# Optimization experiments

Measured on AMD Instinct MI355X. Metric: run time of the kernel, lower is better.

## Reference

```python
import jax, jax.numpy as jnp
import numpy as np

DEGREE = 7

def setup_inputs() -> dict:
    key = jax.random.key(0)
    k1, k2 = jax.random.split(key)
    input_dims, output_dims = 1024, 1024
    x = jax.random.normal(k1, (8192, input_dims), dtype=jnp.float32)
    std = 1.0 / (input_dims * (DEGREE + 1))
    lucas_coeffs = std * jax.random.normal(k2, (input_dims, output_dims, DEGREE + 1), dtype=jnp.float32)
    return {"x": x, "lucas_coeffs": lucas_coeffs}

def reference(x, lucas_coeffs):
    input_dims = lucas_coeffs.shape[0]
    x = x.reshape(-1, input_dims)
    x = jnp.tanh(x)
    # Lucas polynomial recurrence: L0=2, L1=x, L_i = x*L_{i-1} + L_{i-2}
    basis = [jnp.full_like(x, 2.0)]
    if DEGREE > 0:
        basis.append(x)
    for i in range(2, DEGREE + 1):
        basis.append(x * basis[-1] + basis[-2])
    lucas = jnp.stack(basis, axis=-1)  # [b, i, d]
    y = jnp.einsum('bid,iod->bo', lucas, lucas_coeffs)
    return y
```

## Files before the change

### kernel.cpp

```cpp
#include <hip/hip_runtime.h>
#include <hip/hip_bf16.h>


typedef __attribute__((ext_vector_type(8)))  short  short8;
typedef __attribute__((ext_vector_type(4)))  unsigned short ushort4v;
typedef __attribute__((ext_vector_type(8)))  unsigned short ushort8;
typedef __attribute__((ext_vector_type(4)))  float  float4v;
typedef __attribute__((ext_vector_type(4)))  unsigned int uint4v;

#define M_DIM 8192
#define I_DIM 1024
#define O_DIM 1024
#define K_DIM 8192
#define BM 128
#define BN 128
#define BK 64

__device__ __forceinline__ unsigned short f2bf(float f) {
    unsigned int u = __float_as_uint(f);
    u += 0x7FFFu + ((u >> 16) & 1u);
    return (unsigned short)(u >> 16);
}

__global__ __launch_bounds__(256) void prep_t_kernel(const float* __restrict__ x,
                                                     unsigned short* __restrict__ T) {
    int idx = (blockIdx.x * 256 + threadIdx.x) * 4;
    float4v v = *(const float4v*)(x + idx);
    ushort4v o;
    o[0] = f2bf(tanhf(v[0]));
    o[1] = f2bf(tanhf(v[1]));
    o[2] = f2bf(tanhf(v[2]));
    o[3] = f2bf(tanhf(v[3]));
    *(ushort4v*)(T + idx) = o;
}

__global__ __launch_bounds__(256) void prep_b_kernel(const float* __restrict__ c,
                                                     unsigned short* __restrict__ Bt) {
    int idx = blockIdx.x * 256 + threadIdx.x;
    int i = idx >> 10;
    int o = idx & 1023;
    const float* src = c + (size_t)i * 8192 + o * 8;
    float4v lo = *(const float4v*)(src);
    float4v hi = *(const float4v*)(src + 4);
    ushort8 v;
    v[0] = f2bf(lo[0]); v[1] = f2bf(lo[1]); v[2] = f2bf(lo[2]); v[3] = f2bf(lo[3]);
    v[4] = f2bf(hi[0]); v[5] = f2bf(hi[1]); v[6] = f2bf(hi[2]); v[7] = f2bf(hi[3]);
    *(ushort8*)(Bt + (size_t)o * K_DIM + i * 8) = v;
}

__global__ __launch_bounds__(256, 2) void gemm_kernel(const unsigned short* __restrict__ T,
                                                      const unsigned short* __restrict__ Bt,
                                                      float* __restrict__ out) {
    __shared__ unsigned short As[BM * BK];
    __shared__ unsigned short Bs[2][BN * BK];
    __shared__ unsigned short Ts[2][BM * 8];

    const int tid  = threadIdx.x;
    const int lane = tid & 63;
    const int wave = tid >> 6;
    const int m0 = blockIdx.x * BM;
    const int n0 = blockIdx.y * BN;

    const int wm0  = (wave >> 1) * 64;
    const int wn0  = (wave & 1) * 64;
    const int l16  = lane & 15;
    const int quad = lane >> 4;

    const int srow   = lane >> 3;
    const int il     = lane & 7;
    const int gchunk = il ^ srow;

    float4v acc[4][4];
    const float4v zero = {0.f, 0.f, 0.f, 0.f};
    #pragma unroll
    for (int a = 0; a < 4; ++a)
        #pragma unroll
        for (int b = 0; b < 4; ++b) acc[a][b] = zero;

    #pragma unroll
    for (int r = 0; r < 4; ++r) {
        const int rowb = r * 32 + wave * 8;
        const unsigned short* gB = Bt + (size_t)(n0 + rowb + srow) * K_DIM + gchunk * 8;
        __builtin_amdgcn_global_load_lds(
            (const __attribute__((address_space(1))) unsigned int*)gB,
            (__attribute__((address_space(3))) unsigned int*)&Bs[0][rowb * BK], 16, 0, 0);
    }
    if (wave < 2) {
        const unsigned short* gT = T + (size_t)(m0 + wave * 64 + lane) * I_DIM;
        __builtin_amdgcn_global_load_lds(
            (const __attribute__((address_space(1))) unsigned int*)gT,
            (__attribute__((address_space(3))) unsigned int*)&Ts[0][wave * 64 * 8], 16, 0, 0);
    }
    __syncthreads();

    int cur = 0;
    for (int kt = 0; kt < K_DIM; kt += BK) {
        #pragma unroll
        for (int j = 0; j < 4; ++j) {
            const int row = wave * 32 + j * 8 + srow;
            const unsigned int tb = Ts[cur][row * 8 + il];
            const float t = __uint_as_float(tb << 16);
            const float L2v = fmaf(t, t, 2.0f);
            const float L3v = fmaf(t, L2v, t);
            const float L4v = fmaf(t, L3v, L2v);
            const float L5v = fmaf(t, L4v, L3v);
            const float L6v = fmaf(t, L5v, L4v);
            const float L7v = fmaf(t, L6v, L5v);
            const unsigned int u2 = __float_as_uint(L2v) + 0x8000u;
            const unsigned int u3 = __float_as_uint(L3v) + 0x8000u;
            const unsigned int u4 = __float_as_uint(L4v) + 0x8000u;
            const unsigned int u5 = __float_as_uint(L5v) + 0x8000u;
            const unsigned int u6 = __float_as_uint(L6v) + 0x8000u;
            const unsigned int u7 = __float_as_uint(L7v) + 0x8000u;
            uint4v pk;
            pk[0] = 0x4000u | (tb << 16);
            pk[1] = __builtin_amdgcn_perm(u3, u2, 0x07060302);
            pk[2] = __builtin_amdgcn_perm(u5, u4, 0x07060302);
            pk[3] = __builtin_amdgcn_perm(u7, u6, 0x07060302);
            *(uint4v*)&As[row * BK + ((il ^ srow) * 8)] = pk;
        }
        __syncthreads();

        const int nxt = cur ^ 1;
        if (kt + BK < K_DIM) {
            #pragma unroll
            for (int r = 0; r < 4; ++r) {
                const int rowb = r * 32 + wave * 8;
                const unsigned short* gB = Bt + (size_t)(n0 + rowb + srow) * K_DIM
                                              + (kt + BK) + gchunk * 8;
                __builtin_amdgcn_global_load_lds(
                    (const __attribute__((address_space(1))) unsigned int*)gB,
                    (__attribute__((address_space(3))) unsigned int*)&Bs[nxt][rowb * BK], 16, 0, 0);
            }
            if (wave < 2) {
                const unsigned short* gT = T + (size_t)(m0 + wave * 64 + lane) * I_DIM
                                             + (kt + BK) / 8;
                __builtin_amdgcn_global_load_lds(
                    (const __attribute__((address_space(1))) unsigned int*)gT,
                    (__attribute__((address_space(3))) unsigned int*)&Ts[nxt][wave * 64 * 8], 16, 0, 0);
            }
        }

        #pragma unroll
        for (int k2 = 0; k2 < 2; ++k2) {
            short8 af[4], bfr[4];
            #pragma unroll
            for (int t = 0; t < 4; ++t) {
                const int arow = wm0 + t * 16 + l16;
                af[t]  = *(const short8*)&As[arow * BK + (((k2 * 4 + quad) ^ (l16 & 7)) * 8)];
                const int brow = wn0 + t * 16 + l16;
                bfr[t] = *(const short8*)&Bs[cur][brow * BK + (((k2 * 4 + quad) ^ (l16 & 7)) * 8)];
            }
            #pragma unroll
            for (int tm = 0; tm < 4; ++tm)
                #pragma unroll
                for (int tn = 0; tn < 4; ++tn)
                    acc[tm][tn] = __builtin_amdgcn_mfma_f32_16x16x32_bf16(
                        af[tm], bfr[tn], acc[tm][tn], 0, 0, 0);
        }
        __syncthreads();
        cur = nxt;
    }

    #pragma unroll
    for (int tm = 0; tm < 4; ++tm) {
        #pragma unroll
        for (int tn = 0; tn < 4; ++tn) {
            const int col = n0 + wn0 + tn * 16 + l16;
            #pragma unroll
            for (int r = 0; r < 4; ++r) {
                const int row = m0 + wm0 + tm * 16 + quad * 4 + r;
                out[(size_t)row * O_DIM + col] = acc[tm][tn][r];
            }
        }
    }
}

__global__ __launch_bounds__(256) void naive_kernel(const float* __restrict__ x,
                                                    const float* __restrict__ c,
                                                    float* __restrict__ out) {
    int idx = blockIdx.x * 256 + threadIdx.x;
    int b = idx >> 10;
    int o = idx & 1023;
    const float* xb = x + (size_t)b * I_DIM;
    float acc = 0.f;
    for (int i = 0; i < I_DIM; ++i) {
        float t = tanhf(xb[i]);
        float L[8];
        L[0] = 2.0f; L[1] = t;
        #pragma unroll
        for (int d = 2; d < 8; ++d) L[d] = t * L[d - 1] + L[d - 2];
        const float* cc = c + (size_t)i * 8192 + o * 8;
        #pragma unroll
        for (int d = 0; d < 8; ++d) acc += L[d] * cc[d];
    }
    out[idx] = acc;
}

extern "C" void kernel_launch(void* const* d_in, const int* in_sizes, int n_in,
                              void* d_out, int out_size, void* d_ws, size_t ws_size,
                              hipStream_t stream) {
    const float* x      = (const float*)d_in[0];
    const float* coeffs = (const float*)d_in[1];
    float* out = (float*)d_out;

    const size_t btBytes = (size_t)O_DIM * K_DIM * sizeof(unsigned short);
    const size_t tBytes  = (size_t)M_DIM * I_DIM * sizeof(unsigned short);

    if (ws_size >= btBytes + tBytes) {
        unsigned short* Bt = (unsigned short*)d_ws;
        unsigned short* T  = (unsigned short*)((char*)d_ws + btBytes);

        prep_b_kernel<<<(I_DIM * O_DIM) / 256, 256, 0, stream>>>(coeffs, Bt);
        prep_t_kernel<<<(M_DIM * I_DIM) / (4 * 256), 256, 0, stream>>>(x, T);

        dim3 grid(M_DIM / BM, O_DIM / BN);
        gemm_kernel<<<grid, 256, 0, stream>>>(T, Bt, out);
    } else {
        naive_kernel<<<(M_DIM * O_DIM) / 256, 256, 0, stream>>>(x, coeffs, out);
    }
}
```

Before: 259.2 us.

## Build Lucas A-fragments in registers and shrink the GEMM M-tile

The Lucas basis A-operand is now computed straight into MFMA fragments in registers from the staged tanh values, so the As shared buffer, its writes, and one barrier per K step are gone. BM drops from 128 to 64 with a 2x4 accumulator tile per wave, and launch bounds rise to allow 4 blocks per CU. The cost is redundant polynomial evaluation, since each wave recomputes its A fragments for both halves of the N-tile. Halving BM also doubles the number of times the B tile is loaded from global memory and lowers MFMA reuse per LDS read.

```diff
diff --git a/kernel.cpp b/kernel.cpp
--- a/kernel.cpp
+++ b/kernel.cpp
@@ -12,9 +12,10 @@
 #define I_DIM 1024
 #define O_DIM 1024
 #define K_DIM 8192
-#define BM 128
+#define BM 64
 #define BN 128
 #define BK 64
+#define NSTEP (K_DIM / BK)
 
 __device__ __forceinline__ unsigned short f2bf(float f) {
     unsigned int u = __float_as_uint(f);
@@ -48,10 +49,31 @@
     *(ushort8*)(Bt + (size_t)o * K_DIM + i * 8) = v;
 }
 
-__global__ __launch_bounds__(256, 2) void gemm_kernel(const unsigned short* __restrict__ T,
+__device__ __forceinline__ short8 lucas_frag(unsigned int tb) {
+    const float t = __uint_as_float(tb << 16);
+    const float L2v = fmaf(t, t, 2.0f);
+    const float L3v = fmaf(t, L2v, t);
+    const float L4v = fmaf(t, L3v, L2v);
+    const float L5v = fmaf(t, L4v, L3v);
+    const float L6v = fmaf(t, L5v, L4v);
+    const float L7v = fmaf(t, L6v, L5v);
+    const unsigned int u2 = __float_as_uint(L2v) + 0x8000u;
+    const unsigned int u3 = __float_as_uint(L3v) + 0x8000u;
+    const unsigned int u4 = __float_as_uint(L4v) + 0x8000u;
+    const unsigned int u5 = __float_as_uint(L5v) + 0x8000u;
+    const unsigned int u6 = __float_as_uint(L6v) + 0x8000u;
+    const unsigned int u7 = __float_as_uint(L7v) + 0x8000u;
+    union { uint4v u; short8 s; } r;
+    r.u[0] = 0x4000u | (tb << 16);
+    r.u[1] = __builtin_amdgcn_perm(u3, u2, 0x07060302);
+    r.u[2] = __builtin_amdgcn_perm(u5, u4, 0x07060302);
+    r.u[3] = __builtin_amdgcn_perm(u7, u6, 0x07060302);
+    return r.s;
+}
+
+__global__ __launch_bounds__(256, 4) void gemm_kernel(const unsigned short* __restrict__ T,
                                                       const unsigned short* __restrict__ Bt,
                                                       float* __restrict__ out) {
-    __shared__ unsigned short As[BM * BK];
     __shared__ unsigned short Bs[2][BN * BK];
     __shared__ unsigned short Ts[2][BM * 8];
 
@@ -61,7 +83,7 @@
     const int m0 = blockIdx.x * BM;
     const int n0 = blockIdx.y * BN;
 
-    const int wm0  = (wave >> 1) * 64;
+    const int wm0  = (wave >> 1) * 32;
     const int wn0  = (wave & 1) * 64;
     const int l16  = lane & 15;
     const int quad = lane >> 4;
@@ -70,10 +92,10 @@
     const int il     = lane & 7;
     const int gchunk = il ^ srow;
 
-    float4v acc[4][4];
+    float4v acc[2][4];
     const float4v zero = {0.f, 0.f, 0.f, 0.f};
     #pragma unroll
-    for (int a = 0; a < 4; ++a)
+    for (int a = 0; a < 2; ++a)
         #pragma unroll
         for (int b = 0; b < 4; ++b) acc[a][b] = zero;
 
@@ -85,92 +107,75 @@
             (const __attribute__((address_space(1))) unsigned int*)gB,
             (__attribute__((address_space(3))) unsigned int*)&Bs[0][rowb * BK], 16, 0, 0);
     }
-    if (wave < 2) {
-        const unsigned short* gT = T + (size_t)(m0 + wave * 64 + lane) * I_DIM;
+    if (wave == 0) {
+        const unsigned short* gT = T + (size_t)(m0 + lane) * I_DIM;
         __builtin_amdgcn_global_load_lds(
             (const __attribute__((address_space(1))) unsigned int*)gT,
-            (__attribute__((address_space(3))) unsigned int*)&Ts[0][wave * 64 * 8], 16, 0, 0);
+            (__attribute__((address_space(3))) unsigned int*)&Ts[0][0], 16, 0, 0);
     }
     __syncthreads();
 
     int cur = 0;
-    for (int kt = 0; kt < K_DIM; kt += BK) {
-        #pragma unroll
-        for (int j = 0; j < 4; ++j) {
-            const int row = wave * 32 + j * 8 + srow;
-            const unsigned int tb = Ts[cur][row * 8 + il];
-            const float t = __uint_as_float(tb << 16);
-            const float L2v = fmaf(t, t, 2.0f);
-            const float L3v = fmaf(t, L2v, t);
-            const float L4v = fmaf(t, L3v, L2v);
-            const float L5v = fmaf(t, L4v, L3v);
-            const float L6v = fmaf(t, L5v, L4v);
-            const float L7v = fmaf(t, L6v, L5v);
-            const unsigned int u2 = __float_as_uint(L2v) + 0x8000u;
-            const unsigned int u3 = __float_as_uint(L3v) + 0x8000u;
-            const unsigned int u4 = __float_as_uint(L4v) + 0x8000u;
-            const unsigned int u5 = __float_as_uint(L5v) + 0x8000u;
-            const unsigned int u6 = __float_as_uint(L6v) + 0x8000u;
-            const unsigned int u7 = __float_as_uint(L7v) + 0x8000u;
-            uint4v pk;
-            pk[0] = 0x4000u | (tb << 16);
-            pk[1] = __builtin_amdgcn_perm(u3, u2, 0x07060302);
-            pk[2] = __builtin_amdgcn_perm(u5, u4, 0x07060302);
-            pk[3] = __builtin_amdgcn_perm(u7, u6, 0x07060302);
-            *(uint4v*)&As[row * BK + ((il ^ srow) * 8)] = pk;
-        }
-        __syncthreads();
-
+    for (int s = 0; s < NSTEP; ++s) {
         const int nxt = cur ^ 1;
-        if (kt + BK < K_DIM) {
+
+        if (s + 1 < NSTEP) {
+            const int kt = (s + 1) * BK;
             #pragma unroll
             for (int r = 0; r < 4; ++r) {
                 const int rowb = r * 32 + wave * 8;
-                const unsigned short* gB = Bt + (size_t)(n0 + rowb + srow) * K_DIM
-                                              + (kt + BK) + gchunk * 8;
+                const unsigned short* gB = Bt + (size_t)(n0 + rowb + srow) * K_DIM + kt + gchunk * 8;
                 __builtin_amdgcn_global_load_lds(
                     (const __attribute__((address_space(1))) unsigned int*)gB,
                     (__attribute__((address_space(3))) unsigned int*)&Bs[nxt][rowb * BK], 16, 0, 0);
             }
-            if (wave < 2) {
-                const unsigned short* gT = T + (size_t)(m0 + wave * 64 + lane) * I_DIM
-                                             + (kt + BK) / 8;
+            if (wave == 0) {
+                const unsigned short* gT = T + (size_t)(m0 + lane) * I_DIM + kt / 8;
                 __builtin_amdgcn_global_load_lds(
                     (const __attribute__((address_space(1))) unsigned int*)gT,
-                    (__attribute__((address_space(3))) unsigned int*)&Ts[nxt][wave * 64 * 8], 16, 0, 0);
+                    (__attribute__((address_space(3))) unsigned int*)&Ts[nxt][0], 16, 0, 0);
             }
         }
 
+        unsigned int tb[2][2];
+        #pragma unroll
+        for (int tt = 0; tt < 2; ++tt)
+            #pragma unroll
+            for (int k2 = 0; k2 < 2; ++k2)
+                tb[tt][k2] = Ts[cur][(wm0 + tt * 16 + l16) * 8 + (k2 * 4 + quad)];
+
         #pragma unroll
         for (int k2 = 0; k2 < 2; ++k2) {
-            short8 af[4], bfr[4];
-            #pragma unroll
-            for (int t = 0; t < 4; ++t) {
-                const int arow = wm0 + t * 16 + l16;
-                af[t]  = *(const short8*)&As[arow * BK + (((k2 * 4 + quad) ^ (l16 & 7)) * 8)];
-                const int brow = wn0 + t * 16 + l16;
-                bfr[t] = *(const short8*)&Bs[cur][brow * BK + (((k2 * 4 + quad) ^ (l16 & 7)) * 8)];
-            }
-            #pragma unroll
-            for (int tm = 0; tm < 4; ++tm)
+            short8 af[2];
+            af[0] = lucas_frag(tb[0][k2]);
+            af[1] = lucas_frag(tb[1][k2]);
+            short8 bfr[4];
+            #pragma unroll
+            for (int tn = 0; tn < 4; ++tn) {
+                const int brow = wn0 + tn * 16 + l16;
+                bfr[tn] = *(const short8*)&Bs[cur][brow * BK + (((k2 * 4 + quad) ^ (l16 & 7)) * 8)];
+            }
+            #pragma unroll
+            for (int tt = 0; tt < 2; ++tt)
                 #pragma unroll
                 for (int tn = 0; tn < 4; ++tn)
-                    acc[tm][tn] = __builtin_amdgcn_mfma_f32_16x16x32_bf16(
-                        af[tm], bfr[tn], acc[tm][tn], 0, 0, 0);
+                    acc[tt][tn] = __builtin_amdgcn_mfma_f32_16x16x32_bf16(
+                        af[tt], bfr[tn], acc[tt][tn], 0, 0, 0);
         }
+
         __syncthreads();
         cur = nxt;
     }
 
     #pragma unroll
-    for (int tm = 0; tm < 4; ++tm) {
+    for (int tt = 0; tt < 2; ++tt) {
         #pragma unroll
         for (int tn = 0; tn < 4; ++tn) {
             const int col = n0 + wn0 + tn * 16 + l16;
             #pragma unroll
             for (int r = 0; r < 4; ++r) {
-                const int row = m0 + wm0 + tm * 16 + quad * 4 + r;
-                out[(size_t)row * O_DIM + col] = acc[tm][tn][r];
+                const int row = m0 + wm0 + tt * 16 + quad * 4 + r;
+                out[(size_t)row * O_DIM + col] = acc[tt][tn][r];
             }
         }
     }
```

Measured after the change: 268.5 us. 3.6% more time.
